# Performance work log

Measured on AMD Instinct MI355X. Metric: run time of the kernel, lower is better.

Reference implementation:

```python
import jax, jax.numpy as jnp
import numpy as np

B, S, IN = 1, 50000, 128
N = B * S
E = 800000
HID, HEADS, OUT = 64, 2, 64
NEG_SLOPE = 0.2
BN_EPS = 1e-5


def setup_inputs() -> dict:
    key = jax.random.key(0)
    ks = jax.random.split(key, 12)
    s = 0.1
    return {
        "data": jax.random.normal(ks[0], (B, S, IN), jnp.float32),
        "edge_index": jax.random.randint(ks[1], (2, E), 0, N, dtype=jnp.int64),
        "W0": jax.random.normal(ks[2], (IN, HEADS * HID), jnp.float32) * s,
        "att_src0": jax.random.normal(ks[3], (HEADS, HID), jnp.float32) * s,
        "att_dst0": jax.random.normal(ks[4], (HEADS, HID), jnp.float32) * s,
        "bias0": jnp.zeros((HEADS * HID,), jnp.float32),
        "gamma0": jnp.ones((HEADS * HID,), jnp.float32),
        "beta0": jnp.zeros((HEADS * HID,), jnp.float32),
        "W1": jax.random.normal(ks[5], (HEADS * HID, OUT), jnp.float32) * s,
        "att_src1": jax.random.normal(ks[6], (1, OUT), jnp.float32) * s,
        "att_dst1": jax.random.normal(ks[7], (1, OUT), jnp.float32) * s,
        "bias1": jnp.zeros((OUT,), jnp.float32),
    }


def gat_conv(x, edge_index, W, att_src, att_dst, bias, heads, ch, concat):
    n = x.shape[0]
    loop = jnp.arange(n, dtype=edge_index.dtype)
    src = jnp.concatenate([edge_index[0], loop])  # PyG adds self-loops by default
    dst = jnp.concatenate([edge_index[1], loop])
    h = (x @ W).reshape(n, heads, ch)  # [N,H,C]
    a_src = (h * att_src).sum(-1)  # [N,H]
    a_dst = (h * att_dst).sum(-1)  # [N,H]
    e = jax.nn.leaky_relu(a_src[src] + a_dst[dst], NEG_SLOPE)  # [Etot,H]
    m = jax.ops.segment_max(e, dst, num_segments=n)  # segment softmax over dst
    ex = jnp.exp(e - m[dst])
    denom = jax.ops.segment_sum(ex, dst, num_segments=n)
    alpha = ex / (denom[dst] + 1e-16)  # [Etot,H]
    out = jax.ops.segment_sum(h[src] * alpha[:, :, None], dst, num_segments=n)  # [N,H,C]
    out = out.reshape(n, heads * ch) if concat else out.mean(axis=1)
    return out + bias


def reference(data, edge_index, W0, att_src0, att_dst0, bias0, gamma0, beta0,
              W1, att_src1, att_dst1, bias1):
    x = data.reshape(N, IN)
    x = gat_conv(x, edge_index, W0, att_src0, att_dst0, bias0, HEADS, HID, True)
    mu = x.mean(axis=0)
    var = x.var(axis=0)
    x = (x - mu) * jax.lax.rsqrt(var + BN_EPS) * gamma0 + beta0  # BatchNorm1d (batch stats)
    x = jax.nn.elu(x)
    x = gat_conv(x, edge_index, W1, att_src1, att_dst1, bias1, 1, OUT, False)
    return x.reshape(B, S, OUT)
```

## Files before the change

kernel.cpp:

```cpp
#include <hip/hip_runtime.h>
#include <hip/hip_fp16.h>
#include <math.h>

#define N_NODES 50000
#define E_EDGES 800000
#define NEG_SLOPE 0.2f
#define BN_EPS 1e-5f

#define BK_SHIFT 9
#define NBK 98
#define L1_BLOCKS 256
#define L1_CHUNK (E_EDGES / L1_BLOCKS)
#define CNT_N (NBK * L1_BLOCKS)
#define SCG_BLOCKS ((CNT_N + 1023) / 1024)
#define STAGE_MAX 9216

typedef __attribute__((ext_vector_type(8))) _Float16 half8;
typedef __attribute__((ext_vector_type(4))) float f32x4;

__device__ __forceinline__ float lrelu(float v) { return v > 0.f ? v : NEG_SLOPE * v; }

__global__ void k_zero(float* __restrict__ bn_sum, float* __restrict__ bn_sumsq) {
  int t = threadIdx.x;
  if (t < 128) { bn_sum[t] = 0.f; bn_sumsq[t] = 0.f; }
}

__global__ void k_cvtW(const float* __restrict__ W0, const float* __restrict__ W1,
                       _Float16* __restrict__ W0t, _Float16* __restrict__ W1t) {
  int t = threadIdx.x;
  for (int idx = t; idx < 128 * 128; idx += 256) {
    int k = idx >> 7, c = idx & 127;
    W0t[c * 128 + k] = (_Float16)W0[idx];
  }
  for (int idx = t; idx < 128 * 64; idx += 256) {
    int k = idx >> 6, c = idx & 63;
    W1t[c * 128 + k] = (_Float16)W1[idx];
  }
}

__global__ __launch_bounds__(256) void k_l1hist(const int* __restrict__ dst,
                                                int* __restrict__ cnt) {
  __shared__ int lcnt[NBK];
  int t = threadIdx.x;
  if (t < NBK) lcnt[t] = 0;
  __syncthreads();
  int beg = blockIdx.x * L1_CHUNK, end = beg + L1_CHUNK;
  for (int e = beg + t; e < end; e += 256)
    atomicAdd(&lcnt[((unsigned int)dst[e]) >> BK_SHIFT], 1);
  __syncthreads();
  for (int b = t; b < NBK; b += 256) cnt[b * L1_BLOCKS + blockIdx.x] = lcnt[b];
}

__global__ __launch_bounds__(256) void k_scan1g(const int* __restrict__ cnt,
                                                int* __restrict__ tmp,
                                                int* __restrict__ bsums) {
  __shared__ int ts[256];
  int t = threadIdx.x;
  int base = blockIdx.x * 1024 + t * 4;
  int c0 = (base + 0 < CNT_N) ? cnt[base + 0] : 0;
  int c1 = (base + 1 < CNT_N) ? cnt[base + 1] : 0;
  int c2 = (base + 2 < CNT_N) ? cnt[base + 2] : 0;
  int c3 = (base + 3 < CNT_N) ? cnt[base + 3] : 0;
  int s = c0 + c1 + c2 + c3;
  ts[t] = s;
  __syncthreads();
  for (int off = 1; off < 256; off <<= 1) {
    int v = (t >= off) ? ts[t - off] : 0;
    __syncthreads();
    ts[t] += v;
    __syncthreads();
  }
  int excl = ts[t] - s;
  if (t == 255) bsums[blockIdx.x] = ts[255];
  if (base + 0 < CNT_N) tmp[base + 0] = excl;
  if (base + 1 < CNT_N) tmp[base + 1] = excl + c0;
  if (base + 2 < CNT_N) tmp[base + 2] = excl + c0 + c1;
  if (base + 3 < CNT_N) tmp[base + 3] = excl + c0 + c1 + c2;
}

__global__ void k_scan2g(int* __restrict__ bsums) {
  int t = threadIdx.x;
  int orig = (t < SCG_BLOCKS) ? bsums[t] : 0;
  int v = orig;
#pragma unroll
  for (int off = 1; off < 64; off <<= 1) {
    int u = __shfl_up(v, off);
    if (t >= off) v += u;
  }
  if (t < SCG_BLOCKS) bsums[t] = v - orig;
}

__global__ __launch_bounds__(256) void k_l1scatter(const int* __restrict__ src,
                                                   const int* __restrict__ dst,
                                                   const int* __restrict__ tmp,
                                                   const int* __restrict__ bsums,
                                                   unsigned int* __restrict__ binned) {
  __shared__ int cur[NBK];
  int t = threadIdx.x;
  for (int b = t; b < NBK; b += 256) {
    int idx = b * L1_BLOCKS + blockIdx.x;
    cur[b] = tmp[idx] + bsums[idx >> 10];
  }
  __syncthreads();
  int beg = blockIdx.x * L1_CHUNK, end = beg + L1_CHUNK;
  for (int e = beg + t; e < end; e += 256) {
    unsigned int d = (unsigned int)dst[e];
    int b = d >> BK_SHIFT;
    int p = atomicAdd(&cur[b], 1);
    binned[p] = ((unsigned int)src[e] << 16) | d;
  }
}

__global__ void k_bbase(const int* __restrict__ tmp, const int* __restrict__ bsums,
                        int* __restrict__ bucket_base) {
  int b = threadIdx.x;
  if (b < NBK) {
    int idx = b * L1_BLOCKS;
    bucket_base[b] = tmp[idx] + bsums[idx >> 10];
  }
  if (b == NBK) bucket_base[NBK] = E_EDGES;
}

__global__ __launch_bounds__(256) void k_scatter3(const int* __restrict__ bucket_base,
                                                  const unsigned int* __restrict__ binned,
                                                  int* __restrict__ row_ptr,
                                                  int* __restrict__ csr_src) {
  __shared__ int cnt[512];
  __shared__ int staging[STAGE_MAX];
  __shared__ int ts[256];
  int t = threadIdx.x;
  int b = blockIdx.x;
  int lo = b << BK_SHIFT;
  int hi = lo + 512; if (hi > N_NODES) hi = N_NODES;
  int nloc = hi - lo;
  int base = bucket_base[b];
  int end = bucket_base[b + 1];
  cnt[t] = 0; cnt[t + 256] = 0;
  __syncthreads();
  for (int i = base + t; i < end; i += 256)
    atomicAdd(&cnt[(binned[i] & 0xFFFFu) - lo], 1);
  __syncthreads();
  int c0 = cnt[2 * t], c1 = cnt[2 * t + 1];
  int pair = c0 + c1;
  ts[t] = pair;
  __syncthreads();
  for (int off = 1; off < 256; off <<= 1) {
    int v = (t >= off) ? ts[t - off] : 0;
    __syncthreads();
    ts[t] += v;
    __syncthreads();
  }
  int exclp = ts[t] - pair;
  cnt[2 * t] = exclp;
  cnt[2 * t + 1] = exclp + c0;
  if (2 * t < nloc) row_ptr[lo + 2 * t] = base + exclp;
  if (2 * t + 1 < nloc) row_ptr[lo + 2 * t + 1] = base + exclp + c0;
  if (b == NBK - 1 && t == 0) row_ptr[N_NODES] = E_EDGES;
  __syncthreads();
  for (int i = base + t; i < end; i += 256) {
    unsigned int v = binned[i];
    int d = (int)(v & 0xFFFFu) - lo;
    int p = atomicAdd(&cnt[d], 1);
    int s = (int)(v >> 16);
    if (p < STAGE_MAX) staging[p] = s;
    else csr_src[base + p] = s;
  }
  __syncthreads();
  int tot = end - base;
  int lim = tot < STAGE_MAX ? tot : STAGE_MAX;
  for (int k = t; k < lim; k += 256) csr_src[base + k] = staging[k];
}

__global__ __launch_bounds__(256) void k_gemm0m(
    const float* __restrict__ x, const _Float16* __restrict__ Wt,
    const float* __restrict__ att_s, const float* __restrict__ att_d,
    _Float16* __restrict__ h, float* __restrict__ a_src, float* __restrict__ a_dst) {
  int lane = threadIdx.x & 63;
  int wv = threadIdx.x >> 6;
  int row0 = blockIdx.x * 64 + wv * 16;
  int m = lane & 15, kg = lane >> 4;
  int arow = row0 + m;
  int arowc = arow < N_NODES ? arow : N_NODES - 1;
  f32x4 acc[8];
#pragma unroll
  for (int ct = 0; ct < 8; ct++) acc[ct] = (f32x4){0.f, 0.f, 0.f, 0.f};
#pragma unroll
  for (int kc = 0; kc < 4; kc++) {
    const float* xp = &x[(size_t)arowc * 128 + kc * 32 + kg * 8];
    float4 xa = *(const float4*)xp;
    float4 xb = *(const float4*)(xp + 4);
    half8 af = {(_Float16)xa.x, (_Float16)xa.y, (_Float16)xa.z, (_Float16)xa.w,
                (_Float16)xb.x, (_Float16)xb.y, (_Float16)xb.z, (_Float16)xb.w};
#pragma unroll
    for (int ct = 0; ct < 8; ct++) {
      half8 bf = *(const half8*)&Wt[(ct * 16 + m) * 128 + kc * 32 + kg * 8];
      acc[ct] = __builtin_amdgcn_mfma_f32_16x16x32_f16(af, bf, acc[ct], 0, 0, 0);
    }
  }
  float as[8], ad[8];
#pragma unroll
  for (int ct = 0; ct < 8; ct++) { as[ct] = att_s[ct * 16 + m]; ad[ct] = att_d[ct * 16 + m]; }
#pragma unroll
  for (int r = 0; r < 4; r++) {
    int row = row0 + kg * 4 + r;
    bool ok = row < N_NODES;
    float ps0 = 0.f, pd0 = 0.f, ps1 = 0.f, pd1 = 0.f;
#pragma unroll
    for (int ct = 0; ct < 4; ct++) { ps0 += acc[ct][r] * as[ct]; pd0 += acc[ct][r] * ad[ct]; }
#pragma unroll
    for (int ct = 4; ct < 8; ct++) { ps1 += acc[ct][r] * as[ct]; pd1 += acc[ct][r] * ad[ct]; }
#pragma unroll
    for (int msk = 1; msk <= 8; msk <<= 1) {
      ps0 += __shfl_xor(ps0, msk); pd0 += __shfl_xor(pd0, msk);
      ps1 += __shfl_xor(ps1, msk); pd1 += __shfl_xor(pd1, msk);
    }
    if (ok) {
#pragma unroll
      for (int ct = 0; ct < 8; ct++)
        h[(size_t)row * 128 + ct * 16 + m] = (_Float16)acc[ct][r];
      if (m == 0) {
        a_src[row * 2 + 0] = ps0; a_dst[row * 2 + 0] = pd0;
        a_src[row * 2 + 1] = ps1; a_dst[row * 2 + 1] = pd1;
      }
    }
  }
}

__global__ __launch_bounds__(256) void k_gemm1m(
    const float* __restrict__ y, const float* __restrict__ scale,
    const float* __restrict__ shift, const _Float16* __restrict__ Wt,
    const float* __restrict__ att_s, const float* __restrict__ att_d,
    _Float16* __restrict__ h, float* __restrict__ a_src, float* __restrict__ a_dst) {
  int lane = threadIdx.x & 63;
  int wv = threadIdx.x >> 6;
  int row0 = blockIdx.x * 64 + wv * 16;
  int m = lane & 15, kg = lane >> 4;
  int arow = row0 + m;
  int arowc = arow < N_NODES ? arow : N_NODES - 1;
  f32x4 acc[4];
#pragma unroll
  for (int ct = 0; ct < 4; ct++) acc[ct] = (f32x4){0.f, 0.f, 0.f, 0.f};
#pragma unroll
  for (int kc = 0; kc < 4; kc++) {
    int kb = kc * 32 + kg * 8;
    const float* yp = &y[(size_t)arowc * 128 + kb];
    float4 ya = *(const float4*)yp;
    float4 yb = *(const float4*)(yp + 4);
    float4 sa = *(const float4*)&scale[kb], sb = *(const float4*)&scale[kb + 4];
    float4 fa = *(const float4*)&shift[kb], fb = *(const float4*)&shift[kb + 4];
    float v[8];
    v[0] = ya.x * sa.x + fa.x; v[1] = ya.y * sa.y + fa.y;
    v[2] = ya.z * sa.z + fa.z; v[3] = ya.w * sa.w + fa.w;
    v[4] = yb.x * sb.x + fb.x; v[5] = yb.y * sb.y + fb.y;
    v[6] = yb.z * sb.z + fb.z; v[7] = yb.w * sb.w + fb.w;
    half8 af;
#pragma unroll
    for (int j = 0; j < 8; j++) {
      float e = v[j] > 0.f ? v[j] : __expf(v[j]) - 1.f;
      af[j] = (_Float16)e;
    }
#pragma unroll
    for (int ct = 0; ct < 4; ct++) {
      half8 bf = *(const half8*)&Wt[(ct * 16 + m) * 128 + kb];
      acc[ct] = __builtin_amdgcn_mfma_f32_16x16x32_f16(af, bf, acc[ct], 0, 0, 0);
    }
  }
  float as[4], ad[4];
#pragma unroll
  for (int ct = 0; ct < 4; ct++) { as[ct] = att_s[ct * 16 + m]; ad[ct] = att_d[ct * 16 + m]; }
#pragma unroll
  for (int r = 0; r < 4; r++) {
    int row = row0 + kg * 4 + r;
    bool ok = row < N_NODES;
    float ps = 0.f, pd = 0.f;
#pragma unroll
    for (int ct = 0; ct < 4; ct++) { ps += acc[ct][r] * as[ct]; pd += acc[ct][r] * ad[ct]; }
#pragma unroll
    for (int msk = 1; msk <= 8; msk <<= 1) {
      ps += __shfl_xor(ps, msk); pd += __shfl_xor(pd, msk);
    }
    if (ok) {
#pragma unroll
      for (int ct = 0; ct < 4; ct++)
        h[(size_t)row * 64 + ct * 16 + m] = (_Float16)acc[ct][r];
      if (m == 0) { a_src[row] = ps; a_dst[row] = pd; }
    }
  }
}

__global__ __launch_bounds__(256) void k_wts0(
    const int* __restrict__ row_ptr, const int* __restrict__ csr_src,
    const float* __restrict__ a_src, const float* __restrict__ a_dst,
    float2* __restrict__ wts, float2* __restrict__ selfw) {
  int node = (blockIdx.x * blockDim.x + threadIdx.x) >> 6;
  if (node >= N_NODES) return;
  int l = threadIdx.x & 63;
  float ad0 = a_dst[node * 2], ad1 = a_dst[node * 2 + 1];
  float es0 = lrelu(a_src[node * 2] + ad0);
  float es1 = lrelu(a_src[node * 2 + 1] + ad1);
  int beg = row_ptr[node], end = row_ptr[node + 1];
  const float NEGBIG = -3.0e38f;
  float m0 = NEGBIG, s0 = 0.f, m1 = NEGBIG, s1 = 0.f;
  for (int j = beg + l; j < end; j += 64) {
    int s = csr_src[j];
    float e0 = lrelu(a_src[s * 2] + ad0);
    float e1 = lrelu(a_src[s * 2 + 1] + ad1);
    float nm0 = fmaxf(m0, e0);
    s0 = s0 * __expf(m0 - nm0) + __expf(e0 - nm0); m0 = nm0;
    float nm1 = fmaxf(m1, e1);
    s1 = s1 * __expf(m1 - nm1) + __expf(e1 - nm1); m1 = nm1;
  }
#pragma unroll
  for (int msk = 1; msk < 64; msk <<= 1) {
    float om0 = __shfl_xor(m0, msk), os0 = __shfl_xor(s0, msk);
    float nm0 = fmaxf(m0, om0);
    s0 = s0 * __expf(m0 - nm0) + os0 * __expf(om0 - nm0); m0 = nm0;
    float om1 = __shfl_xor(m1, msk), os1 = __shfl_xor(s1, msk);
    float nm1 = fmaxf(m1, om1);
    s1 = s1 * __expf(m1 - nm1) + os1 * __expf(om1 - nm1); m1 = nm1;
  }
  float fm0 = fmaxf(m0, es0);
  float d0 = s0 * __expf(m0 - fm0) + __expf(es0 - fm0);
  float fm1 = fmaxf(m1, es1);
  float d1 = s1 * __expf(m1 - fm1) + __expf(es1 - fm1);
  float inv0 = 1.f / d0, inv1 = 1.f / d1;
  for (int j = beg + l; j < end; j += 64) {
    int s = csr_src[j];
    float e0 = lrelu(a_src[s * 2] + ad0);
    float e1 = lrelu(a_src[s * 2 + 1] + ad1);
    wts[j] = make_float2(__expf(e0 - fm0) * inv0, __expf(e1 - fm1) * inv1);
  }
  if (l == 0) selfw[node] = make_float2(__expf(es0 - fm0) * inv0, __expf(es1 - fm1) * inv1);
}

__global__ __launch_bounds__(256) void k_acc0(
    const int* __restrict__ row_ptr, const int* __restrict__ csr_src,
    const __half* __restrict__ h, const float2* __restrict__ wts,
    const float2* __restrict__ selfw, const float* __restrict__ bias,
    float* __restrict__ out) {
  int node = (blockIdx.x * blockDim.x + threadIdx.x) >> 6;
  if (node >= N_NODES) return;
  int l = threadIdx.x & 63;
  int head = l >> 5;
  int c = l * 2;
  float2 sw = selfw[node];
  float aself = head ? sw.y : sw.x;
  float2 hv = __half22float2(*(const __half2*)&h[(size_t)node * 128 + c]);
  float acc0 = aself * hv.x, acc1 = aself * hv.y;
  float bcc0 = 0.f, bcc1 = 0.f;
  int beg = row_ptr[node], end = row_ptr[node + 1];
  int j = beg;
  for (; j + 4 <= end; j += 4) {
    int s0 = csr_src[j], s1 = csr_src[j + 1], s2 = csr_src[j + 2], s3 = csr_src[j + 3];
    float2 w0 = wts[j], w1 = wts[j + 1], w2 = wts[j + 2], w3 = wts[j + 3];
    float a0 = head ? w0.y : w0.x, a1 = head ? w1.y : w1.x;
    float a2 = head ? w2.y : w2.x, a3 = head ? w3.y : w3.x;
    float2 f0 = __half22float2(*(const __half2*)&h[(size_t)s0 * 128 + c]);
    float2 f1 = __half22float2(*(const __half2*)&h[(size_t)s1 * 128 + c]);
    float2 f2 = __half22float2(*(const __half2*)&h[(size_t)s2 * 128 + c]);
    float2 f3 = __half22float2(*(const __half2*)&h[(size_t)s3 * 128 + c]);
    acc0 += a0 * f0.x + a2 * f2.x;
    bcc0 += a1 * f1.x + a3 * f3.x;
    acc1 += a0 * f0.y + a2 * f2.y;
    bcc1 += a1 * f1.y + a3 * f3.y;
  }
  for (; j < end; j++) {
    int s = csr_src[j];
    float2 w = wts[j];
    float a = head ? w.y : w.x;
    float2 f = __half22float2(*(const __half2*)&h[(size_t)s * 128 + c]);
    acc0 += a * f.x;
    acc1 += a * f.y;
  }
  float2 o;
  o.x = acc0 + bcc0 + bias[c];
  o.y = acc1 + bcc1 + bias[c + 1];
  *(float2*)&out[(size_t)node * 128 + c] = o;
}

__global__ __launch_bounds__(256) void k_bnstats(const float* __restrict__ x,
                                                 float* __restrict__ bn_sum,
                                                 float* __restrict__ bn_sumsq) {
  int f = threadIdx.x & 127;
  int half = threadIdx.x >> 7;
  float s = 0.f, s2 = 0.f;
  for (int r = blockIdx.x * 2 + half; r < N_NODES; r += gridDim.x * 2) {
    float v = x[(size_t)r * 128 + f];
    s += v;
    s2 += v * v;
  }
  __shared__ float ls[256], ls2[256];
  ls[threadIdx.x] = s;
  ls2[threadIdx.x] = s2;
  __syncthreads();
  if (half == 0) {
    atomicAdd(&bn_sum[f], s + ls[f + 128]);
    atomicAdd(&bn_sumsq[f], s2 + ls2[f + 128]);
  }
}

__global__ void k_bnfinal(const float* __restrict__ sum, const float* __restrict__ sumsq,
                          const float* __restrict__ gamma, const float* __restrict__ beta,
                          float* __restrict__ scale, float* __restrict__ shift) {
  int f = threadIdx.x;
  float mu = sum[f] / (float)N_NODES;
  float var = sumsq[f] / (float)N_NODES - mu * mu;
  float sc = gamma[f] * rsqrtf(var + BN_EPS);
  scale[f] = sc;
  shift[f] = beta[f] - mu * sc;
}

__global__ __launch_bounds__(256) void k_wts1(
    const int* __restrict__ row_ptr, const int* __restrict__ csr_src,
    const float* __restrict__ a_src, const float* __restrict__ a_dst,
    float* __restrict__ wts, float* __restrict__ selfw) {
  int node = (blockIdx.x * blockDim.x + threadIdx.x) >> 6;
  if (node >= N_NODES) return;
  int l = threadIdx.x & 63;
  float ad = a_dst[node];
  float es = lrelu(a_src[node] + ad);
  int beg = row_ptr[node], end = row_ptr[node + 1];
  const float NEGBIG = -3.0e38f;
  float m = NEGBIG, s = 0.f;
  for (int j = beg + l; j < end; j += 64) {
    int sn = csr_src[j];
    float e = lrelu(a_src[sn] + ad);
    float nm = fmaxf(m, e);
    s = s * __expf(m - nm) + __expf(e - nm); m = nm;
  }
#pragma unroll
  for (int msk = 1; msk < 64; msk <<= 1) {
    float om = __shfl_xor(m, msk), os = __shfl_xor(s, msk);
    float nm = fmaxf(m, om);
    s = s * __expf(m - nm) + os * __expf(om - nm); m = nm;
  }
  float fm = fmaxf(m, es);
  float d = s * __expf(m - fm) + __expf(es - fm);
  float inv = 1.f / d;
  for (int j = beg + l; j < end; j += 64) {
    int sn = csr_src[j];
    float e = lrelu(a_src[sn] + ad);
    wts[j] = __expf(e - fm) * inv;
  }
  if (l == 0) selfw[node] = __expf(es - fm) * inv;
}

__global__ __launch_bounds__(256) void k_acc1(
    const int* __restrict__ row_ptr, const int* __restrict__ csr_src,
    const __half* __restrict__ h, const float* __restrict__ wts,
    const float* __restrict__ selfw, const float* __restrict__ bias,
    float* __restrict__ out) {
  int node = (blockIdx.x * blockDim.x + threadIdx.x) >> 6;
  if (node >= N_NODES) return;
  int l = threadIdx.x & 63;
  float acc = selfw[node] * __half2float(h[(size_t)node * 64 + l]);
  float bcc = 0.f;
  int beg = row_ptr[node], end = row_ptr[node + 1];
  int j = beg;
  for (; j + 4 <= end; j += 4) {
    int s0 = csr_src[j], s1 = csr_src[j + 1], s2 = csr_src[j + 2], s3 = csr_src[j + 3];
    float a0 = wts[j], a1 = wts[j + 1], a2 = wts[j + 2], a3 = wts[j + 3];
    float f0 = __half2float(h[(size_t)s0 * 64 + l]);
    float f1 = __half2float(h[(size_t)s1 * 64 + l]);
    float f2 = __half2float(h[(size_t)s2 * 64 + l]);
    float f3 = __half2float(h[(size_t)s3 * 64 + l]);
    acc += a0 * f0 + a2 * f2;
    bcc += a1 * f1 + a3 * f3;
  }
  for (; j < end; j++) {
    int s = csr_src[j];
    acc += wts[j] * __half2float(h[(size_t)s * 64 + l]);
  }
  out[(size_t)node * 64 + l] = acc + bcc + bias[l];
}

extern "C" void kernel_launch(void* const* d_in, const int* in_sizes, int n_in,
                              void* d_out, int out_size, void* d_ws, size_t ws_size,
                              hipStream_t stream) {
  const float* data = (const float*)d_in[0];
  const int* ei = (const int*)d_in[1];
  const float* W0 = (const float*)d_in[2];
  const float* att_src0 = (const float*)d_in[3];
  const float* att_dst0 = (const float*)d_in[4];
  const float* bias0 = (const float*)d_in[5];
  const float* gamma0 = (const float*)d_in[6];
  const float* beta0 = (const float*)d_in[7];
  const float* W1 = (const float*)d_in[8];
  const float* att_src1 = (const float*)d_in[9];
  const float* att_dst1 = (const float*)d_in[10];
  const float* bias1 = (const float*)d_in[11];
  float* out = (float*)d_out;

  char* ws = (char*)d_ws;
  size_t off = 0;
  auto alloc = [&](size_t bytes) -> void* {
    void* p = ws + off;
    off = (off + bytes + 255) & ~(size_t)255;
    return p;
  };
  int* cnt = (int*)alloc((size_t)CNT_N * 4);
  int* tmp = (int*)alloc((size_t)CNT_N * 4);
  int* bsums = (int*)alloc(32 * 4);
  int* bucket_base = (int*)alloc((NBK + 1) * 4);
  int* row_ptr = (int*)alloc((N_NODES + 1) * 4);
  unsigned int* binned = (unsigned int*)alloc((size_t)E_EDGES * 4);
  int* csr_src = (int*)alloc((size_t)E_EDGES * 4);
  _Float16* W0t = (_Float16*)alloc(128 * 128 * 2);
  _Float16* W1t = (_Float16*)alloc(64 * 128 * 2);
  _Float16* h0 = (_Float16*)alloc((size_t)N_NODES * 128 * 2);
  float* a_s0 = (float*)alloc((size_t)N_NODES * 2 * 4);
  float* a_d0 = (float*)alloc((size_t)N_NODES * 2 * 4);
  float2* wts0 = (float2*)alloc((size_t)E_EDGES * 8);
  float2* selfw0 = (float2*)alloc((size_t)N_NODES * 8);
  float* out0 = (float*)alloc((size_t)N_NODES * 128 * 4);
  float* bn_sum = (float*)alloc(128 * 4);
  float* bn_sumsq = (float*)alloc(128 * 4);
  float* bn_scale = (float*)alloc(128 * 4);
  float* bn_shift = (float*)alloc(128 * 4);
  _Float16* h1 = h0;
  float* a_s1 = a_s0;
  float* a_d1 = a_d0;
  float* wts1 = (float*)wts0;
  float* selfw1 = (float*)selfw0;

  const int* srcArr = ei;
  const int* dstArr = ei + E_EDGES;

  k_zero<<<1, 128, 0, stream>>>(bn_sum, bn_sumsq);
  k_cvtW<<<1, 256, 0, stream>>>(W0, W1, W0t, W1t);
  k_l1hist<<<L1_BLOCKS, 256, 0, stream>>>(dstArr, cnt);
  k_scan1g<<<SCG_BLOCKS, 256, 0, stream>>>(cnt, tmp, bsums);
  k_scan2g<<<1, 64, 0, stream>>>(bsums);
  k_l1scatter<<<L1_BLOCKS, 256, 0, stream>>>(srcArr, dstArr, tmp, bsums, binned);
  k_bbase<<<1, 128, 0, stream>>>(tmp, bsums, bucket_base);
  k_scatter3<<<NBK, 256, 0, stream>>>(bucket_base, binned, row_ptr, csr_src);
  k_gemm0m<<<(N_NODES + 63) / 64, 256, 0, stream>>>(data, W0t, att_src0, att_dst0, h0, a_s0,
                                                    a_d0);
  k_wts0<<<(N_NODES + 3) / 4, 256, 0, stream>>>(row_ptr, csr_src, a_s0, a_d0, wts0, selfw0);
  k_acc0<<<(N_NODES + 3) / 4, 256, 0, stream>>>(row_ptr, csr_src, (const __half*)h0, wts0,
                                                selfw0, bias0, out0);
  k_bnstats<<<1024, 256, 0, stream>>>(out0, bn_sum, bn_sumsq);
  k_bnfinal<<<1, 128, 0, stream>>>(bn_sum, bn_sumsq, gamma0, beta0, bn_scale, bn_shift);
  k_gemm1m<<<(N_NODES + 63) / 64, 256, 0, stream>>>(out0, bn_scale, bn_shift, W1t, att_src1,
                                                    att_dst1, h1, a_s1, a_d1);
  k_wts1<<<(N_NODES + 3) / 4, 256, 0, stream>>>(row_ptr, csr_src, a_s1, a_d1, wts1, selfw1);
  k_acc1<<<(N_NODES + 3) / 4, 256, 0, stream>>>(row_ptr, csr_src, (const __half*)h1, wts1,
                                                selfw1, bias1, out);
}
```

Measured before the change: 345.4 us.

## Store attention weights in fp16 and gather rows with 16-byte vector loads

Attention weights for both layers are now written as half precision instead of float, which halves their storage and traffic. The two aggregation kernels are restructured so each lane loads 8 fp16 features at once with a 16-byte vector load. Each wavefront processes 4 (layer 0) or 8 (layer 1) edges in parallel and then reduces the partial sums across lanes with shuffles. The wider loads and parallel edges should cut gather instruction count and raise memory-level parallelism, at the cost of cross-lane reductions, lanes idling on low-degree nodes, and reduced weight precision.

```diff
diff --git a/kernel.cpp b/kernel.cpp
--- a/kernel.cpp
+++ b/kernel.cpp
@@ -291,7 +291,7 @@
 __global__ __launch_bounds__(256) void k_wts0(
     const int* __restrict__ row_ptr, const int* __restrict__ csr_src,
     const float* __restrict__ a_src, const float* __restrict__ a_dst,
-    float2* __restrict__ wts, float2* __restrict__ selfw) {
+    __half2* __restrict__ wts, float2* __restrict__ selfw) {
   int node = (blockIdx.x * blockDim.x + threadIdx.x) >> 6;
   if (node >= N_NODES) return;
   int l = threadIdx.x & 63;
@@ -328,54 +328,65 @@
     int s = csr_src[j];
     float e0 = lrelu(a_src[s * 2] + ad0);
     float e1 = lrelu(a_src[s * 2 + 1] + ad1);
-    wts[j] = make_float2(__expf(e0 - fm0) * inv0, __expf(e1 - fm1) * inv1);
+    wts[j] = __floats2half2_rn(__expf(e0 - fm0) * inv0, __expf(e1 - fm1) * inv1);
   }
   if (l == 0) selfw[node] = make_float2(__expf(es0 - fm0) * inv0, __expf(es1 - fm1) * inv1);
 }
 
 __global__ __launch_bounds__(256) void k_acc0(
     const int* __restrict__ row_ptr, const int* __restrict__ csr_src,
-    const __half* __restrict__ h, const float2* __restrict__ wts,
+    const _Float16* __restrict__ h, const __half2* __restrict__ wts,
     const float2* __restrict__ selfw, const float* __restrict__ bias,
     float* __restrict__ out) {
   int node = (blockIdx.x * blockDim.x + threadIdx.x) >> 6;
   if (node >= N_NODES) return;
   int l = threadIdx.x & 63;
-  int head = l >> 5;
-  int c = l * 2;
-  float2 sw = selfw[node];
-  float aself = head ? sw.y : sw.x;
-  float2 hv = __half22float2(*(const __half2*)&h[(size_t)node * 128 + c]);
-  float acc0 = aself * hv.x, acc1 = aself * hv.y;
-  float bcc0 = 0.f, bcc1 = 0.f;
+  int cl = l & 15, ew = l >> 4;
+  int cbase = cl * 8;
+  int head = cl >> 3;
+  float acc[8];
+#pragma unroll
+  for (int k = 0; k < 8; k++) acc[k] = 0.f;
   int beg = row_ptr[node], end = row_ptr[node + 1];
-  int j = beg;
-  for (; j + 4 <= end; j += 4) {
-    int s0 = csr_src[j], s1 = csr_src[j + 1], s2 = csr_src[j + 2], s3 = csr_src[j + 3];
-    float2 w0 = wts[j], w1 = wts[j + 1], w2 = wts[j + 2], w3 = wts[j + 3];
-    float a0 = head ? w0.y : w0.x, a1 = head ? w1.y : w1.x;
-    float a2 = head ? w2.y : w2.x, a3 = head ? w3.y : w3.x;
-    float2 f0 = __half22float2(*(const __half2*)&h[(size_t)s0 * 128 + c]);
-    float2 f1 = __half22float2(*(const __half2*)&h[(size_t)s1 * 128 + c]);
-    float2 f2 = __half22float2(*(const __half2*)&h[(size_t)s2 * 128 + c]);
-    float2 f3 = __half22float2(*(const __half2*)&h[(size_t)s3 * 128 + c]);
-    acc0 += a0 * f0.x + a2 * f2.x;
-    bcc0 += a1 * f1.x + a3 * f3.x;
-    acc1 += a0 * f0.y + a2 * f2.y;
-    bcc1 += a1 * f1.y + a3 * f3.y;
-  }
-  for (; j < end; j++) {
-    int s = csr_src[j];
-    float2 w = wts[j];
-    float a = head ? w.y : w.x;
-    float2 f = __half22float2(*(const __half2*)&h[(size_t)s * 128 + c]);
-    acc0 += a * f.x;
-    acc1 += a * f.y;
-  }
-  float2 o;
-  o.x = acc0 + bcc0 + bias[c];
-  o.y = acc1 + bcc1 + bias[c + 1];
-  *(float2*)&out[(size_t)node * 128 + c] = o;
+  if (ew == 0) {
+    float2 sw = selfw[node];
+    float a = head ? sw.y : sw.x;
+    half8 hv = *(const half8*)&h[(size_t)node * 128 + cbase];
+#pragma unroll
+    for (int k = 0; k < 8; k++) acc[k] += a * (float)hv[k];
+  }
+  int j = beg + ew;
+  for (; j + 4 < end; j += 8) {
+    int s0 = csr_src[j], s1 = csr_src[j + 4];
+    __half2 w0 = wts[j], w1 = wts[j + 4];
+    half8 h0v = *(const half8*)&h[(size_t)s0 * 128 + cbase];
+    half8 h1v = *(const half8*)&h[(size_t)s1 * 128 + cbase];
+    float a0 = head ? __high2float(w0) : __low2float(w0);
+    float a1 = head ? __high2float(w1) : __low2float(w1);
+#pragma unroll
+    for (int k = 0; k < 8; k++) acc[k] += a0 * (float)h0v[k] + a1 * (float)h1v[k];
+  }
+  if (j < end) {
+    int s0 = csr_src[j];
+    __half2 w0 = wts[j];
+    half8 h0v = *(const half8*)&h[(size_t)s0 * 128 + cbase];
+    float a0 = head ? __high2float(w0) : __low2float(w0);
+#pragma unroll
+    for (int k = 0; k < 8; k++) acc[k] += a0 * (float)h0v[k];
+  }
+#pragma unroll
+  for (int k = 0; k < 8; k++) {
+    acc[k] += __shfl_xor(acc[k], 16);
+    acc[k] += __shfl_xor(acc[k], 32);
+  }
+  if (ew == 0) {
+    float4 b0 = *(const float4*)&bias[cbase];
+    float4 b1 = *(const float4*)&bias[cbase + 4];
+    float4 o0 = make_float4(acc[0] + b0.x, acc[1] + b0.y, acc[2] + b0.z, acc[3] + b0.w);
+    float4 o1 = make_float4(acc[4] + b1.x, acc[5] + b1.y, acc[6] + b1.z, acc[7] + b1.w);
+    *(float4*)&out[(size_t)node * 128 + cbase] = o0;
+    *(float4*)&out[(size_t)node * 128 + cbase + 4] = o1;
+  }
 }
 
 __global__ __launch_bounds__(256) void k_bnstats(const float* __restrict__ x,
@@ -413,7 +424,7 @@
 __global__ __launch_bounds__(256) void k_wts1(
     const int* __restrict__ row_ptr, const int* __restrict__ csr_src,
     const float* __restrict__ a_src, const float* __restrict__ a_dst,
-    float* __restrict__ wts, float* __restrict__ selfw) {
+    __half* __restrict__ wts, float* __restrict__ selfw) {
   int node = (blockIdx.x * blockDim.x + threadIdx.x) >> 6;
   if (node >= N_NODES) return;
   int l = threadIdx.x & 63;
@@ -440,38 +451,61 @@
   for (int j = beg + l; j < end; j += 64) {
     int sn = csr_src[j];
     float e = lrelu(a_src[sn] + ad);
-    wts[j] = __expf(e - fm) * inv;
+    wts[j] = __float2half_rn(__expf(e - fm) * inv);
   }
   if (l == 0) selfw[node] = __expf(es - fm) * inv;
 }
 
 __global__ __launch_bounds__(256) void k_acc1(
     const int* __restrict__ row_ptr, const int* __restrict__ csr_src,
-    const __half* __restrict__ h, const float* __restrict__ wts,
+    const _Float16* __restrict__ h, const __half* __restrict__ wts,
     const float* __restrict__ selfw, const float* __restrict__ bias,
     float* __restrict__ out) {
   int node = (blockIdx.x * blockDim.x + threadIdx.x) >> 6;
   if (node >= N_NODES) return;
   int l = threadIdx.x & 63;
-  float acc = selfw[node] * __half2float(h[(size_t)node * 64 + l]);
-  float bcc = 0.f;
+  int cl = l & 7, ew = l >> 3;
+  int cbase = cl * 8;
+  float acc[8];
+#pragma unroll
+  for (int k = 0; k < 8; k++) acc[k] = 0.f;
   int beg = row_ptr[node], end = row_ptr[node + 1];
-  int j = beg;
-  for (; j + 4 <= end; j += 4) {
-    int s0 = csr_src[j], s1 = csr_src[j + 1], s2 = csr_src[j + 2], s3 = csr_src[j + 3];
-    float a0 = wts[j], a1 = wts[j + 1], a2 = wts[j + 2], a3 = wts[j + 3];
-    float f0 = __half2float(h[(size_t)s0 * 64 + l]);
-    float f1 = __half2float(h[(size_t)s1 * 64 + l]);
-    float f2 = __half2float(h[(size_t)s2 * 64 + l]);
-    float f3 = __half2float(h[(size_t)s3 * 64 + l]);
-    acc += a0 * f0 + a2 * f2;
-    bcc += a1 * f1 + a3 * f3;
-  }
-  for (; j < end; j++) {
-    int s = csr_src[j];
-    acc += wts[j] * __half2float(h[(size_t)s * 64 + l]);
-  }
-  out[(size_t)node * 64 + l] = acc + bcc + bias[l];
+  if (ew == 0) {
+    float a = selfw[node];
+    half8 hv = *(const half8*)&h[(size_t)node * 64 + cbase];
+#pragma unroll
+    for (int k = 0; k < 8; k++) acc[k] += a * (float)hv[k];
+  }
+  int j = beg + ew;
+  for (; j + 8 < end; j += 16) {
+    int s0 = csr_src[j], s1 = csr_src[j + 8];
+    float a0 = __half2float(wts[j]), a1 = __half2float(wts[j + 8]);
+    half8 h0v = *(const half8*)&h[(size_t)s0 * 64 + cbase];
+    half8 h1v = *(const half8*)&h[(size_t)s1 * 64 + cbase];
+#pragma unroll
+    for (int k = 0; k < 8; k++) acc[k] += a0 * (float)h0v[k] + a1 * (float)h1v[k];
+  }
+  if (j < end) {
+    int s0 = csr_src[j];
+    float a0 = __half2float(wts[j]);
+    half8 h0v = *(const half8*)&h[(size_t)s0 * 64 + cbase];
+#pragma unroll
+    for (int k = 0; k < 8; k++) acc[k] += a0 * (float)h0v[k];
+  }
+#pragma unroll
+  for (int k = 0; k < 8; k++) {
+    acc[k] += __shfl_xor(acc[k], 8);
+    acc[k] += __shfl_xor(acc[k], 16);
+    acc[k] += __shfl_xor(acc[k], 32);
+  }
+  if (ew == 0) {
+    float4 b0 = *(const float4*)&bias[cbase];
+    float4 b1 = *(const float4*)&bias[cbase + 4];
+    float4 o0 = make_float4(acc[0] + b0.x, acc[1] + b0.y, acc[2] + b0.z, acc[3] + b0.w);
+    float4 o1 = make_float4(acc[4] + b1.x, acc[5] + b1.y, acc[6] + b1.z, acc[7] + b1.w);
+    *(float4*)&out[(size_t)node * 64 + cbase] = o0;
+    *(float4*)&out[(size_t)node * 64 + cbase + 4] = o1;
+  }
 }
 
 extern "C" void kernel_launch(void* const* d_in, const int* in_sizes, int n_in,
@@ -510,7 +544,7 @@
   _Float16* h0 = (_Float16*)alloc((size_t)N_NODES * 128 * 2);
   float* a_s0 = (float*)alloc((size_t)N_NODES * 2 * 4);
   float* a_d0 = (float*)alloc((size_t)N_NODES * 2 * 4);
-  float2* wts0 = (float2*)alloc((size_t)E_EDGES * 8);
+  __half2* wts0 = (__half2*)alloc((size_t)E_EDGES * 4);
   float2* selfw0 = (float2*)alloc((size_t)N_NODES * 8);
   float* out0 = (float*)alloc((size_t)N_NODES * 128 * 4);
   float* bn_sum = (float*)alloc(128 * 4);
@@ -520,7 +554,7 @@
   _Float16* h1 = h0;
   float* a_s1 = a_s0;
   float* a_d1 = a_d0;
-  float* wts1 = (float*)wts0;
+  __half* wts1 = (__half*)wts0;
   float* selfw1 = (float*)selfw0;
 
   const int* srcArr = ei;
@@ -537,13 +571,11 @@
   k_gemm0m<<<(N_NODES + 63) / 64, 256, 0, stream>>>(data, W0t, att_src0, att_dst0, h0, a_s0,
                                                     a_d0);
   k_wts0<<<(N_NODES + 3) / 4, 256, 0, stream>>>(row_ptr, csr_src, a_s0, a_d0, wts0, selfw0);
-  k_acc0<<<(N_NODES + 3) / 4, 256, 0, stream>>>(row_ptr, csr_src, (const __half*)h0, wts0,
-                                                selfw0, bias0, out0);
+  k_acc0<<<(N_NODES + 3) / 4, 256, 0, stream>>>(row_ptr, csr_src, h0, wts0, selfw0, bias0, out0);
   k_bnstats<<<1024, 256, 0, stream>>>(out0, bn_sum, bn_sumsq);
   k_bnfinal<<<1, 128, 0, stream>>>(bn_sum, bn_sumsq, gamma0, beta0, bn_scale, bn_shift);
   k_gemm1m<<<(N_NODES + 63) / 64, 256, 0, stream>>>(out0, bn_scale, bn_shift, W1t, att_src1,
                                                     att_dst1, h1, a_s1, a_d1);
   k_wts1<<<(N_NODES + 3) / 4, 256, 0, stream>>>(row_ptr, csr_src, a_s1, a_d1, wts1, selfw1);
-  k_acc1<<<(N_NODES + 3) / 4, 256, 0, stream>>>(row_ptr, csr_src, (const __half*)h1, wts1,
-                                                selfw1, bias1, out);
-}
+  k_acc1<<<(N_NODES + 3) / 4, 256, 0, stream>>>(row_ptr, csr_src, h1, wts1, selfw1, bias1, out);
+}
```

New measurement: 330.3 us. 1.05x faster.
